# Optimization experiments

Measured on AMD Instinct MI355X. Metric: run time of the kernel, lower is better.

## Reference

```python
import jax, jax.numpy as jnp
import numpy as np

H = 1024          # hidden_dim
E = 8             # num_experts
TOP_K = 2
FF = 4 * H        # ExpertFFN inner dim (standard transformer FFN assumption)
B, S = 2, 2048


def setup_inputs() -> dict:
    key = jax.random.key(0)
    ks = jax.random.split(key, 12)
    std = 0.02 / np.sqrt(H)
    return {
        "x": jax.random.normal(ks[0], (B, S, H), dtype=jnp.float32),
        "gate_w": jax.random.normal(ks[1], (E, H), dtype=jnp.float32) * std,  # nn.Linear weight [out,in]
        "gate_b": jnp.zeros((E,), dtype=jnp.float32),                          # self.bias param
        # routed experts, stacked: FFN = W2 @ gelu(W1 @ x + b1) + b2
        "w1": jax.random.normal(ks[2], (E, H, FF), dtype=jnp.float32) * (1.0 / np.sqrt(H)),
        "b1": jnp.zeros((E, FF), dtype=jnp.float32),
        "w2": jax.random.normal(ks[3], (E, FF, H), dtype=jnp.float32) * (1.0 / np.sqrt(FF)),
        "b2": jnp.zeros((E, H), dtype=jnp.float32),
        # shared expert
        "sw1": jax.random.normal(ks[4], (H, FF), dtype=jnp.float32) * (1.0 / np.sqrt(H)),
        "sb1": jnp.zeros((FF,), dtype=jnp.float32),
        "sw2": jax.random.normal(ks[5], (FF, H), dtype=jnp.float32) * (1.0 / np.sqrt(FF)),
        "sb2": jnp.zeros((H,), dtype=jnp.float32),
    }


def _moe_forward(x, gate_w, gate_b, w1, b1, w2, b2, sw1, sb1, sw2, sb2):
    b, s, h = x.shape
    xf = x.reshape(-1, h)                                    # [T, H]
    # sigmoid gating with learned bias (aux-loss-free load balancing bias)
    scores = jax.nn.sigmoid(xf @ gate_w.T + gate_b)          # [T, E]
    top_scores, top_idx = jax.lax.top_k(scores, TOP_K)       # [T, k]
    top_scores = top_scores / (top_scores.sum(-1, keepdims=True) + 1e-6)
    # per-expert combine weights: sum of normalized scores over top-k slots
    comb = (jax.nn.one_hot(top_idx, E, dtype=xf.dtype) * top_scores[..., None]).sum(1)  # [T, E]
    # dense grouped FFN over all experts (reference; faithful math to masked dispatch)
    hdn = jax.nn.gelu(jnp.einsum('th,ehf->etf', xf, w1) + b1[:, None, :], approximate=False)
    y = jnp.einsum('etf,efh->eth', hdn, w2) + b2[:, None, :]  # [E, T, H]
    routed = jnp.einsum('te,eth->th', comb, y)                # [T, H]
    shared = (jax.nn.gelu(xf @ sw1 + sb1, approximate=False) @ sw2 + sb2) * 0.1
    return (routed + shared).reshape(b, s, h)                 # dropout: eval mode (identity)


def reference(x, gate_w, gate_b, w1, b1, w2, b2, sw1, sb1, sw2, sb2):
    return _moe_forward(x, gate_w, gate_b, w1, b1, w2, b2, sw1, sb1, sw2, sb2)
```

## Files before the change

kernel.cpp:

```cpp
#include <hip/hip_runtime.h>
#include <stdint.h>

#define H_DIM 1024
#define E_NUM 8
#define FF_DIM 4096
#define T_TOK 4096
#define MAX_MT 104

typedef __bf16 bf16x8 __attribute__((ext_vector_type(8)));
typedef float f32x4 __attribute__((ext_vector_type(4)));

#define AS1 __attribute__((address_space(1)))
#define AS3 __attribute__((address_space(3)))

__device__ __forceinline__ unsigned short f2bf(float f) {
  union { float f; uint32_t u; } v; v.f = f;
  uint32_t u = v.u;
  uint32_t r = u + 0x7fffu + ((u >> 16) & 1u);
  return (unsigned short)(r >> 16);
}

__device__ __forceinline__ float gelu_f(float x) {
  float s = x * x;
  float g = x * (1.5957691216f + 0.0713548162f * s);
  float t = __expf(-g);
  return x * __builtin_amdgcn_rcpf(1.0f + t);
}

__global__ __launch_bounds__(64) void gate_kernel(
    const float* __restrict__ x, const float* __restrict__ gw, const float* __restrict__ gb,
    int* __restrict__ topidx, float* __restrict__ topw, int* __restrict__ counts) {
  int t = blockIdx.x;
  int l = threadIdx.x;
  const float* xt = x + (size_t)t * H_DIM;
  float acc[E_NUM];
  #pragma unroll
  for (int e = 0; e < E_NUM; e++) acc[e] = 0.f;
  for (int k = l; k < H_DIM; k += 64) {
    float xv = xt[k];
    #pragma unroll
    for (int e = 0; e < E_NUM; e++) acc[e] += xv * gw[e * H_DIM + k];
  }
  #pragma unroll
  for (int e = 0; e < E_NUM; e++) {
    float v = acc[e];
    #pragma unroll
    for (int off = 32; off > 0; off >>= 1) v += __shfl_xor(v, off, 64);
    acc[e] = v;
  }
  if (l == 0) {
    float s[E_NUM];
    #pragma unroll
    for (int e = 0; e < E_NUM; e++) s[e] = 1.f / (1.f + __expf(-(acc[e] + gb[e])));
    int i1 = 0; float v1 = s[0];
    #pragma unroll
    for (int e = 1; e < E_NUM; e++) if (s[e] > v1) { v1 = s[e]; i1 = e; }
    int i2 = -1; float v2 = -1.f;
    #pragma unroll
    for (int e = 0; e < E_NUM; e++) if (e != i1 && s[e] > v2) { v2 = s[e]; i2 = e; }
    float denom = v1 + v2 + 1e-6f;
    topidx[t * 2]     = i1; topidx[t * 2 + 1] = i2;
    topw[t * 2]       = v1 / denom;
    topw[t * 2 + 1]   = v2 / denom;
    atomicAdd(&counts[i1], 1);
    atomicAdd(&counts[i2], 1);
  }
}

__global__ void init_kernel(int* counts) {
  if (threadIdx.x < E_NUM) counts[threadIdx.x] = 0;
}

__global__ void scan_kernel(const int* __restrict__ counts, int* __restrict__ offs,
                            int* __restrict__ cursor, int* __restrict__ tmE,
                            int* __restrict__ tmM, int* __restrict__ tmCnt) {
  if (threadIdx.x == 0) {
    int a = 0;
    for (int e = 0; e < E_NUM; e++) { offs[e] = a; a += counts[e]; cursor[e] = 0; }
    offs[E_NUM] = a;
    offs[E_NUM + 1] = a + T_TOK;
    int c = 0;
    for (int e = 0; e <= E_NUM; e++) {
      int cnt = (e < E_NUM) ? counts[e] : T_TOK;
      for (int m0 = 0; m0 < cnt; m0 += 128) { tmE[c] = e; tmM[c] = m0; c++; }
    }
    tmCnt[0] = c;
  }
}

__global__ void dispatch_kernel(const int* __restrict__ topidx, const float* __restrict__ topw,
                                const int* __restrict__ offs, int* __restrict__ cursor,
                                int* __restrict__ gidx, int* __restrict__ slot_of) {
  int t = blockIdx.x * blockDim.x + threadIdx.x;
  if (t >= T_TOK) return;
  #pragma unroll
  for (int j = 0; j < 2; j++) {
    int ex  = topidx[t * 2 + j];
    int pos = atomicAdd(&cursor[ex], 1);
    int slot = offs[ex] + pos;
    gidx[slot] = t;
    slot_of[t * 2 + j] = slot;
  }
  gidx[2 * T_TOK + t] = t;
}

__global__ __launch_bounds__(256) void cast_x_kernel(const float* __restrict__ x,
                                                     unsigned short* __restrict__ xb) {
  int i = blockIdx.x * blockDim.x + threadIdx.x;
  float4 v = ((const float4*)x)[i];
  ushort4 o;
  o.x = f2bf(v.x); o.y = f2bf(v.y); o.z = f2bf(v.z); o.w = f2bf(v.w);
  ((ushort4*)xb)[i] = o;
}

__global__ __launch_bounds__(256) void transpose_cast_kernel(
    const float* __restrict__ in, unsigned short* __restrict__ out, int R, int C) {
  __shared__ float tile[64][65];
  const size_t bo = (size_t)blockIdx.z * (size_t)R * C;
  const float* inb = in + bo;
  unsigned short* outb = out + bo;
  int c0 = blockIdx.x * 64, r0 = blockIdx.y * 64;
  int tx = threadIdx.x & 15, ty = threadIdx.x >> 4;
  #pragma unroll
  for (int i = 0; i < 4; i++) {
    int row = ty + i * 16;
    float4 v = *(const float4*)(inb + (size_t)(r0 + row) * C + c0 + tx * 4);
    tile[row][tx * 4 + 0] = v.x;
    tile[row][tx * 4 + 1] = v.y;
    tile[row][tx * 4 + 2] = v.z;
    tile[row][tx * 4 + 3] = v.w;
  }
  __syncthreads();
  int rr0 = tx * 4;
  #pragma unroll
  for (int p = 0; p < 4; p++) {
    int col = p * 16 + ty;
    ushort4 o;
    o.x = f2bf(tile[rr0 + 0][col]);
    o.y = f2bf(tile[rr0 + 1][col]);
    o.z = f2bf(tile[rr0 + 2][col]);
    o.w = f2bf(tile[rr0 + 3][col]);
    *(ushort4*)(outb + (size_t)(c0 + col) * R + r0 + rr0) = o;
  }
}

template <bool FFN1>
__global__ __launch_bounds__(256) void gemm128(
    const unsigned short* __restrict__ A,
    const unsigned short* __restrict__ Bt,
    const float* __restrict__ b_r,
    const float* __restrict__ b_s,
    void* __restrict__ outp,
    const int* __restrict__ gidx,
    const int* __restrict__ offs,
    const int* __restrict__ tmE, const int* __restrict__ tmM,
    const int* __restrict__ tmCnt,
    int K, int N) {
  if ((int)blockIdx.y >= tmCnt[0]) return;

  __shared__ __align__(16) char ldsA[2][128 * 128];
  __shared__ __align__(16) char ldsB[2][128 * 128];
  __shared__ int tokLds[128];

  const int tid = threadIdx.x;
  const int w = tid >> 6;
  const int l = tid & 63;
  const int e  = tmE[blockIdx.y];
  const int m0 = tmM[blockIdx.y];
  const int cnt = offs[e + 1] - offs[e];
  const int base = offs[e] + m0;
  const int valid = min(128, cnt - m0);
  const int n0 = blockIdx.x * 128;

  if (FFN1) {
    if (tid < 128) tokLds[tid] = gidx[base + min(tid, valid - 1)];
    __syncthreads();
  }

  const int lr = l >> 3;
  const int su = (l & 7) ^ lr;
  const unsigned short* aSrc[4];
  const unsigned short* bSrc[4];
  const unsigned short* BtE = Bt + (size_t)e * (size_t)N * (size_t)K;
  #pragma unroll
  for (int i = 0; i < 4; i++) {
    int r = w * 32 + i * 8 + lr;
    size_t arow = FFN1 ? (size_t)tokLds[r] : (size_t)(base + r);
    aSrc[i] = A + arow * (size_t)K + su * 8;
    int rr = r & 63;
    int nr = n0 + (r & 64) + ((rr & 15) << 2) + (rr >> 4);
    bSrc[i] = BtE + (size_t)nr * (size_t)K + su * 8;
  }
  const int dOff = (w * 32 + lr) * 128;

#define STAGE(c, kt)                                                               \
  {                                                                                \
    _Pragma("unroll")                                                              \
    for (int i = 0; i < 4; i++) {                                                  \
      __builtin_amdgcn_global_load_lds((const AS1 void*)(aSrc[i] + (kt) * 64),     \
                                       (AS3 void*)(&ldsA[c][i * 1024 + dOff]),     \
                                       16, 0, 0);                                  \
      __builtin_amdgcn_global_load_lds((const AS1 void*)(bSrc[i] + (kt) * 64),     \
                                       (AS3 void*)(&ldsB[c][i * 1024 + dOff]),     \
                                       16, 0, 0);                                  \
    }                                                                              \
  }

  f32x4 acc[4][4];
  #pragma unroll
  for (int m = 0; m < 4; m++)
    #pragma unroll
    for (int n = 0; n < 4; n++) acc[m][n] = (f32x4){0.f, 0.f, 0.f, 0.f};

  const int wr = w >> 1, wc = w & 1;
  const int l15 = l & 15, l4 = l >> 4, l7 = l & 7;
  const int nt = K >> 6;

  STAGE(0, 0);
  __syncthreads();

  for (int t = 0; t < nt; t++) {
    const int cur = t & 1;
    if (t + 1 < nt) STAGE(cur ^ 1, t + 1);

    const char* pA = &ldsA[cur][0];
    const char* pB = &ldsB[cur][0];
    #pragma unroll
    for (int kk = 0; kk < 2; kk++) {
      const int uoff = ((kk * 4 + l4) ^ l7) << 4;
      bf16x8 af[4], bfr[4];
      #pragma unroll
      for (int m = 0; m < 4; m++)
        af[m] = *(const bf16x8*)(pA + (wr * 64 + m * 16 + l15) * 128 + uoff);
      #pragma unroll
      for (int n = 0; n < 4; n++)
        bfr[n] = *(const bf16x8*)(pB + (wc * 64 + n * 16 + l15) * 128 + uoff);
      #pragma unroll
      for (int m = 0; m < 4; m++)
        #pragma unroll
        for (int n = 0; n < 4; n++)
          acc[m][n] = __builtin_amdgcn_mfma_f32_16x16x32_bf16(af[m], bfr[n], acc[m][n], 0, 0, 0);
    }
    __syncthreads();
  }
#undef STAGE

  const float* bias = (e < E_NUM) ? (b_r + (size_t)e * N) : b_s;
  const int c0 = n0 + wc * 64 + 4 * l15;
  float4 bv = *(const float4*)(bias + c0);
  if (FFN1) {
    unsigned short* hdn = (unsigned short*)outp;
    #pragma unroll
    for (int m = 0; m < 4; m++) {
      #pragma unroll
      for (int j = 0; j < 4; j++) {
        int rl = wr * 64 + m * 16 + l4 * 4 + j;
        if (rl < valid) {
          ushort4 o;
          o.x = f2bf(gelu_f(acc[m][0][j] + bv.x));
          o.y = f2bf(gelu_f(acc[m][1][j] + bv.y));
          o.z = f2bf(gelu_f(acc[m][2][j] + bv.z));
          o.w = f2bf(gelu_f(acc[m][3][j] + bv.w));
          *(ushort4*)(hdn + (size_t)(base + rl) * N + c0) = o;
        }
      }
    }
  } else {
    float* y = (float*)outp;
    #pragma unroll
    for (int m = 0; m < 4; m++) {
      #pragma unroll
      for (int j = 0; j < 4; j++) {
        int rl = wr * 64 + m * 16 + l4 * 4 + j;
        if (rl < valid) {
          float4 o;
          o.x = acc[m][0][j] + bv.x;
          o.y = acc[m][1][j] + bv.y;
          o.z = acc[m][2][j] + bv.z;
          o.w = acc[m][3][j] + bv.w;
          *(float4*)(y + (size_t)(base + rl) * N + c0) = o;
        }
      }
    }
  }
}

__global__ __launch_bounds__(256) void combine_kernel(
    const float* __restrict__ y, const float* __restrict__ topw,
    const int* __restrict__ slot_of, float* __restrict__ out) {
  int t = blockIdx.x;
  int g = threadIdx.x;
  int s1 = slot_of[2 * t], s2 = slot_of[2 * t + 1];
  float w1 = topw[2 * t], w2 = topw[2 * t + 1];
  float4 a = *(const float4*)(y + (size_t)s1 * H_DIM + g * 4);
  float4 b = *(const float4*)(y + (size_t)s2 * H_DIM + g * 4);
  float4 c = *(const float4*)(y + (size_t)(2 * T_TOK + t) * H_DIM + g * 4);
  float4 o;
  o.x = w1 * a.x + w2 * b.x + 0.1f * c.x;
  o.y = w1 * a.y + w2 * b.y + 0.1f * c.y;
  o.z = w1 * a.z + w2 * b.z + 0.1f * c.z;
  o.w = w1 * a.w + w2 * b.w + 0.1f * c.w;
  *(float4*)(out + (size_t)t * H_DIM + g * 4) = o;
}

extern "C" void kernel_launch(void* const* d_in, const int* in_sizes, int n_in,
                              void* d_out, int out_size, void* d_ws, size_t ws_size,
                              hipStream_t stream) {
  const float* x   = (const float*)d_in[0];
  const float* gw  = (const float*)d_in[1];
  const float* gb  = (const float*)d_in[2];
  const float* w1  = (const float*)d_in[3];
  const float* b1  = (const float*)d_in[4];
  const float* w2  = (const float*)d_in[5];
  const float* b2  = (const float*)d_in[6];
  const float* sw1 = (const float*)d_in[7];
  const float* sb1 = (const float*)d_in[8];
  const float* sw2 = (const float*)d_in[9];
  const float* sb2 = (const float*)d_in[10];
  float* out = (float*)d_out;

  char* p = (char*)d_ws;
  auto alloc = [&](size_t bytes) {
    char* r = p;
    p += (bytes + 255) & ~(size_t)255;
    return r;
  };
  int*   counts  = (int*)alloc(E_NUM * 4);
  int*   cursor  = (int*)alloc(E_NUM * 4);
  int*   offs    = (int*)alloc((E_NUM + 2) * 4);
  int*   topidx  = (int*)alloc((size_t)T_TOK * 2 * 4);
  float* topw    = (float*)alloc((size_t)T_TOK * 2 * 4);
  int*   slot_of = (int*)alloc((size_t)T_TOK * 2 * 4);
  int*   gidx    = (int*)alloc((size_t)3 * T_TOK * 4);
  int*   tmE     = (int*)alloc(MAX_MT * 4);
  int*   tmM     = (int*)alloc(MAX_MT * 4);
  int*   tmCnt   = (int*)alloc(4);
  unsigned short* xb   = (unsigned short*)alloc((size_t)T_TOK * H_DIM * 2);
  unsigned short* wAll = (unsigned short*)alloc((size_t)(E_NUM + 1) * FF_DIM * H_DIM * 2);
  unsigned short* hdn  = (unsigned short*)alloc((size_t)3 * T_TOK * FF_DIM * 2);
  float*          yb   = (float*)alloc((size_t)3 * T_TOK * H_DIM * 4);

  init_kernel<<<1, 64, 0, stream>>>(counts);
  gate_kernel<<<T_TOK, 64, 0, stream>>>(x, gw, gb, topidx, topw, counts);
  scan_kernel<<<1, 1, 0, stream>>>(counts, offs, cursor, tmE, tmM, tmCnt);
  dispatch_kernel<<<T_TOK / 256, 256, 0, stream>>>(topidx, topw, offs, cursor, gidx, slot_of);

  cast_x_kernel<<<(T_TOK * H_DIM / 4) / 256, 256, 0, stream>>>(x, xb);

  transpose_cast_kernel<<<dim3(FF_DIM / 64, H_DIM / 64, E_NUM), 256, 0, stream>>>(w1, wAll, H_DIM, FF_DIM);
  transpose_cast_kernel<<<dim3(FF_DIM / 64, H_DIM / 64, 1), 256, 0, stream>>>(
      sw1, wAll + (size_t)E_NUM * FF_DIM * H_DIM, H_DIM, FF_DIM);
  gemm128<true><<<dim3(FF_DIM / 128, MAX_MT), 256, 0, stream>>>(
      xb, wAll, b1, sb1, hdn, gidx, offs, tmE, tmM, tmCnt, H_DIM, FF_DIM);

  transpose_cast_kernel<<<dim3(H_DIM / 64, FF_DIM / 64, E_NUM), 256, 0, stream>>>(w2, wAll, FF_DIM, H_DIM);
  transpose_cast_kernel<<<dim3(H_DIM / 64, FF_DIM / 64, 1), 256, 0, stream>>>(
      sw2, wAll + (size_t)E_NUM * FF_DIM * H_DIM, FF_DIM, H_DIM);
  gemm128<false><<<dim3(H_DIM / 128, MAX_MT), 256, 0, stream>>>(
      hdn, wAll, b2, sb2, yb, gidx, offs, tmE, tmM, tmCnt, FF_DIM, H_DIM);

  combine_kernel<<<T_TOK, 256, 0, stream>>>(yb, topw, slot_of, out);
}
```

Baseline: 594.6 us.

## Pre-gather activations, enlarge GEMM tile to 128x256, store bf16 expert outputs

The GEMM tile grows from 128x128 with 256 threads to 128x256 with 512 threads. This halves how often each A tile is re-read and gives eight waves per block. Token rows are now gathered and cast into a contiguous bf16 buffer in a separate kernel, so the FFN1 GEMM no longer uses an indirect token index. The shared and routed weight transposes are merged into single launches, and the second GEMM writes bf16 instead of fp32 to cut combine traffic. The trade-offs are lower precision in the expert outputs, the extra gather pass, and fewer blocks for FFN2 (N=1024 gives only 4 column tiles).

```diff
diff --git a/kernel.cpp b/kernel.cpp
--- a/kernel.cpp
+++ b/kernel.cpp
@@ -18,6 +18,10 @@
   uint32_t u = v.u;
   uint32_t r = u + 0x7fffu + ((u >> 16) & 1u);
   return (unsigned short)(r >> 16);
+}
+__device__ __forceinline__ float bf2f(unsigned short u) {
+  union { uint32_t u; float f; } v; v.u = ((uint32_t)u) << 16;
+  return v.f;
 }
 
 __device__ __forceinline__ float gelu_f(float x) {
@@ -104,21 +108,25 @@
   gidx[2 * T_TOK + t] = t;
 }
 
-__global__ __launch_bounds__(256) void cast_x_kernel(const float* __restrict__ x,
-                                                     unsigned short* __restrict__ xb) {
-  int i = blockIdx.x * blockDim.x + threadIdx.x;
-  float4 v = ((const float4*)x)[i];
+__global__ __launch_bounds__(256) void gather_x_kernel(
+    const float* __restrict__ x, const int* __restrict__ gidx,
+    unsigned short* __restrict__ xg) {
+  int slot = blockIdx.x;
+  int g = threadIdx.x;
+  int tok = gidx[slot];
+  float4 v = *(const float4*)(x + (size_t)tok * H_DIM + g * 4);
   ushort4 o;
   o.x = f2bf(v.x); o.y = f2bf(v.y); o.z = f2bf(v.z); o.w = f2bf(v.w);
-  ((ushort4*)xb)[i] = o;
-}
-
-__global__ __launch_bounds__(256) void transpose_cast_kernel(
-    const float* __restrict__ in, unsigned short* __restrict__ out, int R, int C) {
+  *(ushort4*)(xg + (size_t)slot * H_DIM + g * 4) = o;
+}
+
+__global__ __launch_bounds__(256) void transpose_cast9_kernel(
+    const float* __restrict__ w, const float* __restrict__ sw,
+    unsigned short* __restrict__ out, int R, int C) {
   __shared__ float tile[64][65];
-  const size_t bo = (size_t)blockIdx.z * (size_t)R * C;
-  const float* inb = in + bo;
-  unsigned short* outb = out + bo;
+  const int z = blockIdx.z;
+  const float* inb = (z < E_NUM) ? (w + (size_t)z * R * C) : sw;
+  unsigned short* outb = out + (size_t)z * R * C;
   int c0 = blockIdx.x * 64, r0 = blockIdx.y * 64;
   int tx = threadIdx.x & 15, ty = threadIdx.x >> 4;
   #pragma unroll
@@ -145,13 +153,12 @@
 }
 
 template <bool FFN1>
-__global__ __launch_bounds__(256) void gemm128(
+__global__ __launch_bounds__(512, 1) void gemm128x256(
     const unsigned short* __restrict__ A,
     const unsigned short* __restrict__ Bt,
     const float* __restrict__ b_r,
     const float* __restrict__ b_s,
-    void* __restrict__ outp,
-    const int* __restrict__ gidx,
+    unsigned short* __restrict__ outp,
     const int* __restrict__ offs,
     const int* __restrict__ tmE, const int* __restrict__ tmM,
     const int* __restrict__ tmCnt,
@@ -159,8 +166,7 @@
   if ((int)blockIdx.y >= tmCnt[0]) return;
 
   __shared__ __align__(16) char ldsA[2][128 * 128];
-  __shared__ __align__(16) char ldsB[2][128 * 128];
-  __shared__ int tokLds[128];
+  __shared__ __align__(16) char ldsB[2][256 * 128];
 
   const int tid = threadIdx.x;
   const int w = tid >> 6;
@@ -170,40 +176,32 @@
   const int cnt = offs[e + 1] - offs[e];
   const int base = offs[e] + m0;
   const int valid = min(128, cnt - m0);
-  const int n0 = blockIdx.x * 128;
-
-  if (FFN1) {
-    if (tid < 128) tokLds[tid] = gidx[base + min(tid, valid - 1)];
-    __syncthreads();
-  }
-
-  const int lr = l >> 3;
-  const int su = (l & 7) ^ lr;
-  const unsigned short* aSrc[4];
-  const unsigned short* bSrc[4];
+  const int n0 = blockIdx.x * 256;
+
+  const int srow = tid >> 3;
+  const int su   = (tid & 7) ^ (srow & 7);
+  const unsigned short* aPtr[2];
+  const unsigned short* bPtr[4];
   const unsigned short* BtE = Bt + (size_t)e * (size_t)N * (size_t)K;
   #pragma unroll
-  for (int i = 0; i < 4; i++) {
-    int r = w * 32 + i * 8 + lr;
-    size_t arow = FFN1 ? (size_t)tokLds[r] : (size_t)(base + r);
-    aSrc[i] = A + arow * (size_t)K + su * 8;
-    int rr = r & 63;
-    int nr = n0 + (r & 64) + ((rr & 15) << 2) + (rr >> 4);
-    bSrc[i] = BtE + (size_t)nr * (size_t)K + su * 8;
-  }
-  const int dOff = (w * 32 + lr) * 128;
+  for (int p = 0; p < 2; p++)
+    aPtr[p] = A + (size_t)(base + p * 64 + srow) * (size_t)K + su * 8;
+  #pragma unroll
+  for (int p = 0; p < 4; p++) {
+    int nr = n0 + p * 64 + ((srow & 15) << 2) + (srow >> 4);
+    bPtr[p] = BtE + (size_t)nr * (size_t)K + su * 8;
+  }
 
 #define STAGE(c, kt)                                                               \
   {                                                                                \
     _Pragma("unroll")                                                              \
-    for (int i = 0; i < 4; i++) {                                                  \
-      __builtin_amdgcn_global_load_lds((const AS1 void*)(aSrc[i] + (kt) * 64),     \
-                                       (AS3 void*)(&ldsA[c][i * 1024 + dOff]),     \
-                                       16, 0, 0);                                  \
-      __builtin_amdgcn_global_load_lds((const AS1 void*)(bSrc[i] + (kt) * 64),     \
-                                       (AS3 void*)(&ldsB[c][i * 1024 + dOff]),     \
-                                       16, 0, 0);                                  \
-    }                                                                              \
+    for (int p = 0; p < 2; p++)                                                    \
+      __builtin_amdgcn_global_load_lds((const AS1 void*)(aPtr[p] + (kt) * 64),     \
+          (AS3 void*)(&ldsA[c][p * 8192 + tid * 16]), 16, 0, 0);                   \
+    _Pragma("unroll")                                                              \
+    for (int p = 0; p < 4; p++)                                                    \
+      __builtin_amdgcn_global_load_lds((const AS1 void*)(bPtr[p] + (kt) * 64),     \
+          (AS3 void*)(&ldsB[c][p * 8192 + tid * 16]), 16, 0, 0);                   \
   }
 
   f32x4 acc[4][4];
@@ -212,7 +210,7 @@
     #pragma unroll
     for (int n = 0; n < 4; n++) acc[m][n] = (f32x4){0.f, 0.f, 0.f, 0.f};
 
-  const int wr = w >> 1, wc = w & 1;
+  const int wr = w >> 2, wc = w & 3;
   const int l15 = l & 15, l4 = l >> 4, l7 = l & 7;
   const int nt = K >> 6;
 
@@ -248,58 +246,45 @@
   const float* bias = (e < E_NUM) ? (b_r + (size_t)e * N) : b_s;
   const int c0 = n0 + wc * 64 + 4 * l15;
   float4 bv = *(const float4*)(bias + c0);
-  if (FFN1) {
-    unsigned short* hdn = (unsigned short*)outp;
-    #pragma unroll
-    for (int m = 0; m < 4; m++) {
-      #pragma unroll
-      for (int j = 0; j < 4; j++) {
-        int rl = wr * 64 + m * 16 + l4 * 4 + j;
-        if (rl < valid) {
-          ushort4 o;
+  #pragma unroll
+  for (int m = 0; m < 4; m++) {
+    #pragma unroll
+    for (int j = 0; j < 4; j++) {
+      int rl = wr * 64 + m * 16 + l4 * 4 + j;
+      if (rl < valid) {
+        ushort4 o;
+        if (FFN1) {
           o.x = f2bf(gelu_f(acc[m][0][j] + bv.x));
           o.y = f2bf(gelu_f(acc[m][1][j] + bv.y));
           o.z = f2bf(gelu_f(acc[m][2][j] + bv.z));
           o.w = f2bf(gelu_f(acc[m][3][j] + bv.w));
-          *(ushort4*)(hdn + (size_t)(base + rl) * N + c0) = o;
+        } else {
+          o.x = f2bf(acc[m][0][j] + bv.x);
+          o.y = f2bf(acc[m][1][j] + bv.y);
+          o.z = f2bf(acc[m][2][j] + bv.z);
+          o.w = f2bf(acc[m][3][j] + bv.w);
         }
+        *(ushort4*)(outp + (size_t)(base + rl) * N + c0) = o;
       }
     }
-  } else {
-    float* y = (float*)outp;
-    #pragma unroll
-    for (int m = 0; m < 4; m++) {
-      #pragma unroll
-      for (int j = 0; j < 4; j++) {
-        int rl = wr * 64 + m * 16 + l4 * 4 + j;
-        if (rl < valid) {
-          float4 o;
-          o.x = acc[m][0][j] + bv.x;
-          o.y = acc[m][1][j] + bv.y;
-          o.z = acc[m][2][j] + bv.z;
-          o.w = acc[m][3][j] + bv.w;
-          *(float4*)(y + (size_t)(base + rl) * N + c0) = o;
-        }
-      }
-    }
   }
 }
 
 __global__ __launch_bounds__(256) void combine_kernel(
-    const float* __restrict__ y, const float* __restrict__ topw,
+    const unsigned short* __restrict__ y, const float* __restrict__ topw,
     const int* __restrict__ slot_of, float* __restrict__ out) {
   int t = blockIdx.x;
   int g = threadIdx.x;
   int s1 = slot_of[2 * t], s2 = slot_of[2 * t + 1];
   float w1 = topw[2 * t], w2 = topw[2 * t + 1];
-  float4 a = *(const float4*)(y + (size_t)s1 * H_DIM + g * 4);
-  float4 b = *(const float4*)(y + (size_t)s2 * H_DIM + g * 4);
-  float4 c = *(const float4*)(y + (size_t)(2 * T_TOK + t) * H_DIM + g * 4);
+  ushort4 a = *(const ushort4*)(y + (size_t)s1 * H_DIM + g * 4);
+  ushort4 b = *(const ushort4*)(y + (size_t)s2 * H_DIM + g * 4);
+  ushort4 c = *(const ushort4*)(y + (size_t)(2 * T_TOK + t) * H_DIM + g * 4);
   float4 o;
-  o.x = w1 * a.x + w2 * b.x + 0.1f * c.x;
-  o.y = w1 * a.y + w2 * b.y + 0.1f * c.y;
-  o.z = w1 * a.z + w2 * b.z + 0.1f * c.z;
-  o.w = w1 * a.w + w2 * b.w + 0.1f * c.w;
+  o.x = w1 * bf2f(a.x) + w2 * bf2f(b.x) + 0.1f * bf2f(c.x);
+  o.y = w1 * bf2f(a.y) + w2 * bf2f(b.y) + 0.1f * bf2f(c.y);
+  o.z = w1 * bf2f(a.z) + w2 * bf2f(b.z) + 0.1f * bf2f(c.z);
+  o.w = w1 * bf2f(a.w) + w2 * bf2f(b.w) + 0.1f * bf2f(c.w);
   *(float4*)(out + (size_t)t * H_DIM + g * 4) = o;
 }
 
@@ -335,29 +320,27 @@
   int*   tmE     = (int*)alloc(MAX_MT * 4);
   int*   tmM     = (int*)alloc(MAX_MT * 4);
   int*   tmCnt   = (int*)alloc(4);
-  unsigned short* xb   = (unsigned short*)alloc((size_t)T_TOK * H_DIM * 2);
+  unsigned short* xg   = (unsigned short*)alloc((size_t)3 * T_TOK * H_DIM * 2);
   unsigned short* wAll = (unsigned short*)alloc((size_t)(E_NUM + 1) * FF_DIM * H_DIM * 2);
   unsigned short* hdn  = (unsigned short*)alloc((size_t)3 * T_TOK * FF_DIM * 2);
-  float*          yb   = (float*)alloc((size_t)3 * T_TOK * H_DIM * 4);
+  unsigned short* yb   = (unsigned short*)alloc((size_t)3 * T_TOK * H_DIM * 2);
 
   init_kernel<<<1, 64, 0, stream>>>(counts);
   gate_kernel<<<T_TOK, 64, 0, stream>>>(x, gw, gb, topidx, topw, counts);
   scan_kernel<<<1, 1, 0, stream>>>(counts, offs, cursor, tmE, tmM, tmCnt);
   dispatch_kernel<<<T_TOK / 256, 256, 0, stream>>>(topidx, topw, offs, cursor, gidx, slot_of);
 
-  cast_x_kernel<<<(T_TOK * H_DIM / 4) / 256, 256, 0, stream>>>(x, xb);
-
-  transpose_cast_kernel<<<dim3(FF_DIM / 64, H_DIM / 64, E_NUM), 256, 0, stream>>>(w1, wAll, H_DIM, FF_DIM);
-  transpose_cast_kernel<<<dim3(FF_DIM / 64, H_DIM / 64, 1), 256, 0, stream>>>(
-      sw1, wAll + (size_t)E_NUM * FF_DIM * H_DIM, H_DIM, FF_DIM);
-  gemm128<true><<<dim3(FF_DIM / 128, MAX_MT), 256, 0, stream>>>(
-      xb, wAll, b1, sb1, hdn, gidx, offs, tmE, tmM, tmCnt, H_DIM, FF_DIM);
-
-  transpose_cast_kernel<<<dim3(H_DIM / 64, FF_DIM / 64, E_NUM), 256, 0, stream>>>(w2, wAll, FF_DIM, H_DIM);
-  transpose_cast_kernel<<<dim3(H_DIM / 64, FF_DIM / 64, 1), 256, 0, stream>>>(
-      sw2, wAll + (size_t)E_NUM * FF_DIM * H_DIM, FF_DIM, H_DIM);
-  gemm128<false><<<dim3(H_DIM / 128, MAX_MT), 256, 0, stream>>>(
-      hdn, wAll, b2, sb2, yb, gidx, offs, tmE, tmM, tmCnt, FF_DIM, H_DIM);
+  gather_x_kernel<<<3 * T_TOK, 256, 0, stream>>>(x, gidx, xg);
+
+  transpose_cast9_kernel<<<dim3(FF_DIM / 64, H_DIM / 64, E_NUM + 1), 256, 0, stream>>>(
+      w1, sw1, wAll, H_DIM, FF_DIM);
+  gemm128x256<true><<<dim3(FF_DIM / 256, MAX_MT), 512, 0, stream>>>(
+      xg, wAll, b1, sb1, hdn, offs, tmE, tmM, tmCnt, H_DIM, FF_DIM);
+
+  transpose_cast9_kernel<<<dim3(H_DIM / 64, FF_DIM / 64, E_NUM + 1), 256, 0, stream>>>(
+      w2, sw2, wAll, FF_DIM, H_DIM);
+  gemm128x256<false><<<dim3(H_DIM / 256, MAX_MT), 512, 0, stream>>>(
+      hdn, wAll, b2, sb2, yb, offs, tmE, tmM, tmCnt, FF_DIM, H_DIM);
 
   combine_kernel<<<T_TOK, 256, 0, stream>>>(yb, topw, slot_of, out);
 }
```

After: 653.3 us. +9.9%, slower.
